# Optimization experiments

Hardware: AMD Instinct MI355X
Metric: run time of the kernel (lower is better)

Reference implementation:

```python
import jax, jax.numpy as jnp
import numpy as np
import math

HIDDEN = 768
HEADS = 12
HEAD_DIM = HIDDEN // HEADS
B, T = 2, 2048


def setup_inputs() -> dict:
    key = jax.random.key(0)
    k1, k2, k3, k4, k5 = jax.random.split(key, 5)
    s = 0.02
    return {
        "x": jax.random.normal(k1, (B, T, HIDDEN), dtype=jnp.float32),
        "mask": jnp.ones((B, T), dtype=jnp.int32),
        "w_qkv": jax.random.normal(k2, (3 * HIDDEN, HIDDEN), dtype=jnp.float32) * s,
        "b_qkv": jnp.zeros((3 * HIDDEN,), dtype=jnp.float32),
        "w_out": jax.random.normal(k3, (HIDDEN, HIDDEN), dtype=jnp.float32) * s,
        "b_out": jnp.zeros((HIDDEN,), dtype=jnp.float32),
    }


def reference(x, mask, w_qkv, b_qkv, w_out, b_out):
    Bv, Tv, C = x.shape
    # torch Linear: y = x @ W.T + b
    qkv = jnp.einsum('btc,oc->bto', x, w_qkv) + b_qkv  # [B,T,3C]
    q, k, v = jnp.split(qkv, 3, axis=-1)
    def to_heads(t):
        return t.reshape(Bv, Tv, HEADS, HEAD_DIM).transpose(0, 2, 1, 3)  # [B,H,T,D]
    q, k, v = to_heads(q), to_heads(k), to_heads(v)
    scale = 1.0 / math.sqrt(HEAD_DIM)
    scores = jnp.einsum('bhqd,bhkd->bhqk', q, k) * scale  # [B,H,T,T]
    m = (mask[:, None, None, :] != 0)  # broadcast over heads and query dim
    scores = jnp.where(m, scores, -jnp.inf)
    probs = jax.nn.softmax(scores, axis=-1)
    # dropout is identity in eval mode
    ctx = jnp.einsum('bhqk,bhkd->bhqd', probs, v)  # [B,H,T,D]
    ctx = ctx.transpose(0, 2, 1, 3).reshape(Bv, Tv, C)
    return jnp.einsum('btc,oc->bto', ctx, w_out) + b_out
```

## Files before the change

### kernel.cpp

```cpp
#include <hip/hip_runtime.h>
#include <hip/hip_bf16.h>


typedef __bf16 bf16;
typedef __attribute__((ext_vector_type(4))) __bf16 bf16x4;
typedef __attribute__((ext_vector_type(8))) __bf16 bf16x8;
typedef __attribute__((ext_vector_type(4))) float f32x4;
typedef __attribute__((ext_vector_type(16))) float f32x16;
typedef __attribute__((ext_vector_type(4))) unsigned u32x4;

#define MFMA16(a, b, c) __builtin_amdgcn_mfma_f32_16x16x32_bf16((a), (b), (c), 0, 0, 0)
#define MFMA32(a, b, c) __builtin_amdgcn_mfma_f32_32x32x16_bf16((a), (b), (c), 0, 0, 0)

static constexpr int BB = 2;
static constexpr int TT = 2048;
static constexpr int CC = 768;
static constexpr int HH = 12;
static constexpr int DD = 64;

union U8 { u32x4 u; bf16x8 b; };

__device__ inline void gload16(const bf16* g, bf16* l) {
  __builtin_amdgcn_global_load_lds((const __attribute__((address_space(1))) void*)g,
                                   (__attribute__((address_space(3))) void*)l, 16, 0, 0);
}

__global__ __launch_bounds__(256) void cvt_all(const float* __restrict__ x,
                                               const float* __restrict__ wq,
                                               const float* __restrict__ wo,
                                               bf16* __restrict__ xb,
                                               bf16* __restrict__ wqb,
                                               bf16* __restrict__ wob) {
  const int CX = BB * TT * CC / 8, CQ = 3 * CC * CC / 8;
  int idx = blockIdx.x * 256 + threadIdx.x;
  const float* s;
  bf16* d;
  int off;
  if (idx < CX) { s = x; d = xb; off = idx; }
  else if (idx < CX + CQ) { s = wq; d = wqb; off = idx - CX; }
  else { s = wo; d = wob; off = idx - CX - CQ; }
  const float4* p = (const float4*)(s + (size_t)off * 8);
  float4 a = p[0], b = p[1];
  bf16x8 r;
  r[0] = (bf16)a.x; r[1] = (bf16)a.y; r[2] = (bf16)a.z; r[3] = (bf16)a.w;
  r[4] = (bf16)b.x; r[5] = (bf16)b.y; r[6] = (bf16)b.z; r[7] = (bf16)b.w;
  *(bf16x8*)(d + (size_t)off * 8) = r;
}

template <typename OT>
__global__ __launch_bounds__(256) void gemm_bt_bf16(const bf16* __restrict__ A,
                                                    const bf16* __restrict__ Bw,
                                                    const float* __restrict__ bias,
                                                    OT* __restrict__ Cmat,
                                                    int M, int N, int K,
                                                    float qs, int qcols) {
  __shared__ bf16 As[128 * 64];
  __shared__ bf16 Bs[128 * 64];
  const int tid = threadIdx.x;
  const int m0 = blockIdx.y * 128, n0 = blockIdx.x * 128;
  const int lane = tid & 63, w = tid >> 6;
  const int wm = (w >> 1) * 64, wn = (w & 1) * 64;
  const int lr = lane & 15;
  const int g4 = lane >> 4;
  const int srow8 = lane >> 3;
  const int scs = ((lane & 7) ^ srow8) * 8;
  f32x4 acc[4][4] = {};
  for (int k0 = 0; k0 < K; k0 += 64) {
    __syncthreads();
#pragma unroll
    for (int s = 0; s < 4; s++) {
      const int rowl = w * 32 + s * 8;
      gload16(A  + (size_t)(m0 + rowl + srow8) * K + k0 + scs, &As[rowl * 64]);
      gload16(Bw + (size_t)(n0 + rowl + srow8) * K + k0 + scs, &Bs[rowl * 64]);
    }
    __syncthreads();
#pragma unroll
    for (int ks = 0; ks < 2; ks++) {
      bf16x8 a[4], b[4];
#pragma unroll
      for (int i = 0; i < 4; i++)
        a[i] = *(const bf16x8*)&As[(wm + i * 16 + lr) * 64 + (((ks * 4 + g4) ^ (lr & 7)) * 8)];
#pragma unroll
      for (int j = 0; j < 4; j++)
        b[j] = *(const bf16x8*)&Bs[(wn + j * 16 + lr) * 64 + (((ks * 4 + g4) ^ (lr & 7)) * 8)];
#pragma unroll
      for (int i = 0; i < 4; i++)
#pragma unroll
        for (int j = 0; j < 4; j++)
          acc[i][j] = MFMA16(a[i], b[j], acc[i][j]);
    }
  }
#pragma unroll
  for (int i = 0; i < 4; i++) {
    const int rbase = m0 + wm + i * 16 + (lane >> 4) * 4;
#pragma unroll
    for (int j = 0; j < 4; j++) {
      const int cidx = n0 + wn + j * 16 + lr;
      const float bv = bias[cidx];
      const float sc = (cidx < qcols) ? qs : 1.0f;
#pragma unroll
      for (int r = 0; r < 4; r++) {
        float v = (acc[i][j][r] + bv) * sc;
        Cmat[(size_t)(rbase + r) * N + cidx] = (OT)v;
      }
    }
  }
}

template <int NS>
__global__ __launch_bounds__(256, 4) void attn_fwd(const bf16* __restrict__ qkv,
                                                   const int* __restrict__ mask,
                                                   bf16* __restrict__ po,
                                                   float* __restrict__ ml,
                                                   bf16* __restrict__ ctx) {
  __shared__ bf16 Ks[2][32 * 64];
  __shared__ bf16 Vt[2][64 * 32];
  const int tid = threadIdx.x, lane = tid & 63, w = tid >> 6;
  const int ln31 = lane & 31, hi = lane >> 5;
  const int cpx = 48 * NS;
  const int bid = blockIdx.x;
  const int wg = (bid & 7) * cpx + (bid >> 3);
  const int qb = wg & 15;
  const int t2 = wg >> 4;
  const int s = t2 % NS;
  const int bh = t2 / NS;
  const int h = bh % HH, b = bh / HH;
  const int q = qb * 128 + w * 32 + ln31;
  const size_t rs = 3 * CC;
  const float NEG = -1.0e30f;
  const int kt0 = s * (TT / NS), kt1 = kt0 + TT / NS;

  bf16x8 qreg[4];
  {
    const bf16* qp = qkv + (size_t)(b * TT + q) * rs + h * DD + hi * 8;
#pragma unroll
    for (int ds = 0; ds < 4; ds++) qreg[ds] = *(const bf16x8*)(qp + ds * 16);
  }

  const bf16* kbase = qkv + (size_t)(b * TT) * rs + CC + h * DD;
  const bf16* vbase = qkv + (size_t)(b * TT) * rs + 2 * CC + h * DD;

  const int kkey = w * 8 + (lane >> 3);
  const int kcs = (lane & 7) ^ (kkey & 7) ^ (kkey >> 3);
  auto stage_k = [&](int buf, int kt) {
    gload16(kbase + (size_t)(kt + kkey) * rs + kcs * 8, &Ks[buf][w * 512]);
  };

  const int vkey = w * 8 + (lane >> 3);
  const int vd0 = (lane & 7) * 8;
  const int vpar = vkey & 1;
  const int vkp = vkey >> 1;
  bf16x8 vreg;
  int mv;
  auto load_v = [&](int kt) {
    vreg = *(const bf16x8*)(vbase + (size_t)(kt + vkey) * rs + vd0);
    mv = mask[b * TT + kt + ln31];
  };
  auto vt_put = [&](int buf, int d, unsigned val) {
    const int cp = (vkp >> 2) ^ (d & 3) ^ ((d >> 2) & 3);
    *(unsigned*)&Vt[buf][d * 32 + cp * 8 + (vkp & 3) * 2] = val;
  };
  auto write_v = [&](int buf) {
    U8 uu; uu.b = vreg;
    const u32x4 wv = uu.u;
    unsigned x0 = vpar ? wv[0] : wv[2];
    unsigned x1 = vpar ? wv[1] : wv[3];
    unsigned r0 = __shfl_xor(x0, 8);
    unsigned r1 = __shfl_xor(x1, 8);
    unsigned a0 = vpar ? r0 : wv[0];
    unsigned a1 = vpar ? r1 : wv[1];
    unsigned b0 = vpar ? wv[2] : r0;
    unsigned b1 = vpar ? wv[3] : r1;
    const int dbase = vd0 + vpar * 4;
    vt_put(buf, dbase + 0, (a0 & 0xffffu) | (b0 << 16));
    vt_put(buf, dbase + 1, (a0 >> 16) | (b0 & 0xffff0000u));
    vt_put(buf, dbase + 2, (a1 & 0xffffu) | (b1 << 16));
    vt_put(buf, dbase + 3, (a1 >> 16) | (b1 & 0xffff0000u));
  };

  stage_k(0, kt0);
  load_v(kt0);
  write_v(0);
  __syncthreads();
  int mvc = mv;

  f32x16 oacc0 = {}, oacc1 = {};
  float m = NEG, l = 0.f;
  const int swr = (ln31 & 7) ^ (ln31 >> 3);
  const int vsw = (ln31 & 3) ^ ((ln31 >> 2) & 3);

  int cur = 0;
  for (int kt = kt0; kt < kt1; kt += 32, cur ^= 1) {
    const bool more = kt + 32 < kt1;
    if (more) { stage_k(cur ^ 1, kt + 32); load_v(kt + 32); }

    f32x16 sacc = {};
    __builtin_amdgcn_s_setprio(1);
#pragma unroll
    for (int ds = 0; ds < 4; ds++) {
      bf16x8 kf = *(const bf16x8*)&Ks[cur][ln31 * 64 + ((ds * 2 + hi) ^ swr) * 8];
      sacc = MFMA32(kf, qreg[ds], sacc);
    }
    __builtin_amdgcn_s_setprio(0);

    const unsigned mw = (unsigned)__ballot(mvc != 0);
    if (mw != 0xffffffffu) {
      const unsigned mwh = mw >> (4 * hi);
#pragma unroll
      for (int r = 0; r < 16; r++) {
        const int key = (r & 3) + 8 * (r >> 2);
        if (!((mwh >> key) & 1)) sacc[r] = NEG;
      }
    }

    float mx = sacc[0];
#pragma unroll
    for (int r = 1; r < 16; r++) mx = fmaxf(mx, sacc[r]);
    mx = fmaxf(mx, __shfl_xor(mx, 32));
    if (!__all(mx - m <= 8.f)) {
      const float al = exp2f(m - mx);
      l *= al;
#pragma unroll
      for (int r = 0; r < 16; r++) { oacc0[r] *= al; oacc1[r] *= al; }
      m = mx;
    }
    float p[16], rsum = 0.f;
#pragma unroll
    for (int r = 0; r < 16; r++) { p[r] = exp2f(sacc[r] - m); rsum += p[r]; }
    rsum += __shfl_xor(rsum, 32);
    l += rsum;

    unsigned pk[8];
#pragma unroll
    for (int i = 0; i < 8; i++)
      asm("v_cvt_pk_bf16_f32 %0, %1, %2" : "=v"(pk[i]) : "v"(p[2 * i]), "v"(p[2 * i + 1]));
    asm volatile("v_permlane32_swap_b32 %0, %1" : "+v"(pk[0]), "+v"(pk[2]));
    asm volatile("v_permlane32_swap_b32 %0, %1" : "+v"(pk[1]), "+v"(pk[3]));
    asm volatile("v_permlane32_swap_b32 %0, %1" : "+v"(pk[4]), "+v"(pk[6]));
    asm volatile("v_permlane32_swap_b32 %0, %1" : "+v"(pk[5]), "+v"(pk[7]));

    __builtin_amdgcn_s_setprio(1);
#pragma unroll
    for (int ks = 0; ks < 2; ks++) {
      U8 uu;
      uu.u = (u32x4){pk[ks * 4 + 0], pk[ks * 4 + 1], pk[ks * 4 + 2], pk[ks * 4 + 3]};
      const bf16x8 pb = uu.b;
      const int cph = ((ks * 2 + hi) ^ vsw) * 8;
      bf16x8 vf0 = *(const bf16x8*)&Vt[cur][ln31 * 32 + cph];
      oacc0 = MFMA32(vf0, pb, oacc0);
      bf16x8 vf1 = *(const bf16x8*)&Vt[cur][(32 + ln31) * 32 + cph];
      oacc1 = MFMA32(vf1, pb, oacc1);
    }
    __builtin_amdgcn_s_setprio(0);

    if (more) write_v(cur ^ 1);
    __syncthreads();
    mvc = mv;
  }

  const float invl = l > 0.f ? 1.0f / l : 0.f;
  const size_t gr = (size_t)(b * TT + q);
  bf16* obase = (NS == 1) ? (ctx + gr * CC + h * DD)
                          : (po + (size_t)s * (BB * TT * CC) + gr * CC + h * DD);
#pragma unroll
  for (int g = 0; g < 4; g++) {
    bf16x4 o0, o1;
#pragma unroll
    for (int j = 0; j < 4; j++) {
      o0[j] = (bf16)(oacc0[4 * g + j] * invl);
      o1[j] = (bf16)(oacc1[4 * g + j] * invl);
    }
    *(bf16x4*)(obase + 8 * g + 4 * hi) = o0;
    *(bf16x4*)(obase + 32 + 8 * g + 4 * hi) = o1;
  }
  if (NS > 1 && hi == 0) {
    float2 v2 = {m, l};
    *(float2*)&ml[(((size_t)s * (BB * TT) + gr) * HH + h) * 2] = v2;
  }
}

template <int NS>
__global__ __launch_bounds__(256) void combine(const bf16* __restrict__ po,
                                               const float* __restrict__ ml,
                                               bf16* __restrict__ ctx) {
  const int idx = blockIdx.x * 256 + threadIdx.x;
  const int row = idx / 96;
  const int rem = idx - row * 96;
  const int h = rem >> 3, d8 = rem & 7;
  float ms[NS], ls[NS];
  float M = -1.0e30f;
#pragma unroll
  for (int s = 0; s < NS; s++) {
    const float2 p2 = *(const float2*)&ml[(((size_t)s * (BB * TT) + row) * HH + h) * 2];
    ms[s] = p2.x; ls[s] = p2.y;
    M = fmaxf(M, p2.x);
  }
  float wgt[NS], wsum = 0.f;
#pragma unroll
  for (int s = 0; s < NS; s++) { wgt[s] = ls[s] * exp2f(ms[s] - M); wsum += wgt[s]; }
  const float inv = wsum > 0.f ? 1.0f / wsum : 0.f;
  float acc[8] = {};
#pragma unroll
  for (int s = 0; s < NS; s++) {
    const float ws = wgt[s] * inv;
    const bf16x8 v = *(const bf16x8*)&po[(size_t)s * (BB * TT * CC) + (size_t)row * CC + h * 64 + d8 * 8];
#pragma unroll
    for (int j = 0; j < 8; j++) acc[j] += ws * (float)v[j];
  }
  bf16x8 o;
#pragma unroll
  for (int j = 0; j < 8; j++) o[j] = (bf16)acc[j];
  *(bf16x8*)&ctx[(size_t)row * CC + h * 64 + d8 * 8] = o;
}

extern "C" void kernel_launch(void* const* d_in, const int* in_sizes, int n_in,
                              void* d_out, int out_size, void* d_ws, size_t ws_size,
                              hipStream_t stream) {
  const float* x     = (const float*)d_in[0];
  const int*   mask  = (const int*)d_in[1];
  const float* w_qkv = (const float*)d_in[2];
  const float* b_qkv = (const float*)d_in[3];
  const float* w_out = (const float*)d_in[4];
  const float* b_out = (const float*)d_in[5];
  float* out = (float*)d_out;

  const int M = BB * TT;
  bf16* qkv = (bf16*)d_ws;
  bf16* xb  = qkv + (size_t)M * 3 * CC;
  bf16* ctx = xb;
  bf16* wob = xb + (size_t)M * CC;
  bf16* wqb = wob + (size_t)CC * CC;
  const size_t PO_OFF = (size_t)((M * 3 * CC) + (M * CC) + (CC * CC)) * 2;
  const size_t PER_SPLIT = (size_t)M * CC * 2 + (size_t)M * HH * 2 * 4;

  int NS = 1;
  if (ws_size >= PO_OFF + 8 * PER_SPLIT) NS = 8;
  else if (ws_size >= PO_OFF + 4 * PER_SPLIT) NS = 4;
  else if (ws_size >= PO_OFF + 2 * PER_SPLIT) NS = 2;

  bf16* po = (bf16*)((char*)d_ws + PO_OFF);
  float* ml = (float*)((char*)d_ws + PO_OFF + (size_t)NS * M * CC * 2);

  const int nchunks = (BB * TT * CC + 3 * CC * CC + CC * CC) / 8;
  cvt_all<<<nchunks / 256, 256, 0, stream>>>(x, w_qkv, w_out, xb, wqb, wob);
  gemm_bt_bf16<bf16><<<dim3(3 * CC / 128, M / 128), 256, 0, stream>>>(
      xb, wqb, b_qkv, qkv, M, 3 * CC, CC, 0.125f * 1.44269504f, CC);
  if (NS == 8) {
    attn_fwd<8><<<dim3(384 * 8), 256, 0, stream>>>(qkv, mask, po, ml, ctx);
    combine<8><<<dim3(M * HH * 8 / 256), 256, 0, stream>>>(po, ml, ctx);
  } else if (NS == 4) {
    attn_fwd<4><<<dim3(384 * 4), 256, 0, stream>>>(qkv, mask, po, ml, ctx);
    combine<4><<<dim3(M * HH * 8 / 256), 256, 0, stream>>>(po, ml, ctx);
  } else if (NS == 2) {
    attn_fwd<2><<<dim3(384 * 2), 256, 0, stream>>>(qkv, mask, po, ml, ctx);
    combine<2><<<dim3(M * HH * 8 / 256), 256, 0, stream>>>(po, ml, ctx);
  } else {
    attn_fwd<1><<<dim3(384), 256, 0, stream>>>(qkv, mask, po, ml, ctx);
  }
  gemm_bt_bf16<float><<<dim3(CC / 128, M / 128), 256, 0, stream>>>(
      ctx, wob, b_out, out, M, CC, CC, 1.0f, 0);
}
```

Baseline: 119.9 us.

## Prepack mask bits, drop split count to four, remap GEMM tiles, use pointer increments

Packs the int mask into 32-bit words inside the conversion kernel, so the attention loop loads one word per tile instead of doing a per-lane mask load and a ballot. Caps the split-K attention at four splits, down from eight, which cuts partial-output traffic and combine work but leaves fewer workgroups for parallelism. The GEMM kernels now remap block IDs in an interleaved order meant to improve L2 locality across XCDs. The attention K/V addresses become incremented pointers rather than being recomputed each iteration.

```diff
diff --git a/kernel.cpp b/kernel.cpp
--- a/kernel.cpp
+++ b/kernel.cpp
@@ -28,9 +28,21 @@
 __global__ __launch_bounds__(256) void cvt_all(const float* __restrict__ x,
                                                const float* __restrict__ wq,
                                                const float* __restrict__ wo,
+                                               const int* __restrict__ mask,
                                                bf16* __restrict__ xb,
                                                bf16* __restrict__ wqb,
-                                               bf16* __restrict__ wob) {
+                                               bf16* __restrict__ wob,
+                                               unsigned* __restrict__ mbits) {
+  if (blockIdx.x == gridDim.x - 1) {
+    const int i = threadIdx.x;
+    if (i < BB * TT / 32) {
+      unsigned wrd = 0;
+#pragma unroll
+      for (int j = 0; j < 32; j++) wrd |= (mask[i * 32 + j] != 0 ? 1u : 0u) << j;
+      mbits[i] = wrd;
+    }
+    return;
+  }
   const int CX = BB * TT * CC / 8, CQ = 3 * CC * CC / 8;
   int idx = blockIdx.x * 256 + threadIdx.x;
   const float* s;
@@ -57,7 +69,10 @@
   __shared__ bf16 As[128 * 64];
   __shared__ bf16 Bs[128 * 64];
   const int tid = threadIdx.x;
-  const int m0 = blockIdx.y * 128, n0 = blockIdx.x * 128;
+  const int lin = blockIdx.x + gridDim.x * blockIdx.y;
+  const int chunk = (gridDim.x * gridDim.y) >> 3;
+  const int wgid = (lin & 7) * chunk + (lin >> 3);
+  const int m0 = (wgid / gridDim.x) * 128, n0 = (wgid % gridDim.x) * 128;
   const int lane = tid & 63, w = tid >> 6;
   const int wm = (w >> 1) * 64, wn = (w & 1) * 64;
   const int lr = lane & 15;
@@ -109,7 +124,7 @@
 
 template <int NS>
 __global__ __launch_bounds__(256, 4) void attn_fwd(const bf16* __restrict__ qkv,
-                                                   const int* __restrict__ mask,
+                                                   const unsigned* __restrict__ mbits,
                                                    bf16* __restrict__ po,
                                                    float* __restrict__ ml,
                                                    bf16* __restrict__ ctx) {
@@ -128,7 +143,8 @@
   const int q = qb * 128 + w * 32 + ln31;
   const size_t rs = 3 * CC;
   const float NEG = -1.0e30f;
-  const int kt0 = s * (TT / NS), kt1 = kt0 + TT / NS;
+  const int kt0 = s * (TT / NS);
+  const int NT = (TT / NS) / 32;
 
   bf16x8 qreg[4];
   {
@@ -137,25 +153,18 @@
     for (int ds = 0; ds < 4; ds++) qreg[ds] = *(const bf16x8*)(qp + ds * 16);
   }
 
-  const bf16* kbase = qkv + (size_t)(b * TT) * rs + CC + h * DD;
-  const bf16* vbase = qkv + (size_t)(b * TT) * rs + 2 * CC + h * DD;
-
   const int kkey = w * 8 + (lane >> 3);
   const int kcs = (lane & 7) ^ (kkey & 7) ^ (kkey >> 3);
-  auto stage_k = [&](int buf, int kt) {
-    gload16(kbase + (size_t)(kt + kkey) * rs + kcs * 8, &Ks[buf][w * 512]);
-  };
+  const bf16* kpt = qkv + (size_t)(b * TT + kt0 + kkey) * rs + CC + h * DD + kcs * 8;
 
   const int vkey = w * 8 + (lane >> 3);
   const int vd0 = (lane & 7) * 8;
   const int vpar = vkey & 1;
   const int vkp = vkey >> 1;
+  const bf16* vpt = qkv + (size_t)(b * TT + kt0 + vkey) * rs + 2 * CC + h * DD + vd0;
+  const size_t stride = (size_t)32 * rs;
+
   bf16x8 vreg;
-  int mv;
-  auto load_v = [&](int kt) {
-    vreg = *(const bf16x8*)(vbase + (size_t)(kt + vkey) * rs + vd0);
-    mv = mask[b * TT + kt + ln31];
-  };
   auto vt_put = [&](int buf, int d, unsigned val) {
     const int cp = (vkp >> 2) ^ (d & 3) ^ ((d >> 2) & 3);
     *(unsigned*)&Vt[buf][d * 32 + cp * 8 + (vkp & 3) * 2] = val;
@@ -178,11 +187,14 @@
     vt_put(buf, dbase + 3, (a1 >> 16) | (b1 & 0xffff0000u));
   };
 
-  stage_k(0, kt0);
-  load_v(kt0);
+  const int mbase = (b * TT + kt0) >> 5;
+  unsigned mwc = mbits[mbase];
+
+  gload16(kpt, &Ks[0][w * 512]);
+  vreg = *(const bf16x8*)vpt;
   write_v(0);
+  kpt += stride; vpt += stride;
   __syncthreads();
-  int mvc = mv;
 
   f32x16 oacc0 = {}, oacc1 = {};
   float m = NEG, l = 0.f;
@@ -190,9 +202,15 @@
   const int vsw = (ln31 & 3) ^ ((ln31 >> 2) & 3);
 
   int cur = 0;
-  for (int kt = kt0; kt < kt1; kt += 32, cur ^= 1) {
-    const bool more = kt + 32 < kt1;
-    if (more) { stage_k(cur ^ 1, kt + 32); load_v(kt + 32); }
+  for (int it = 0; it < NT; ++it, cur ^= 1) {
+    const bool more = (it + 1 < NT);
+    unsigned mwn = 0xffffffffu;
+    if (more) {
+      gload16(kpt, &Ks[cur ^ 1][w * 512]);
+      vreg = *(const bf16x8*)vpt;
+      kpt += stride; vpt += stride;
+      mwn = mbits[mbase + it + 1];
+    }
 
     f32x16 sacc = {};
     __builtin_amdgcn_s_setprio(1);
@@ -203,13 +221,11 @@
     }
     __builtin_amdgcn_s_setprio(0);
 
-    const unsigned mw = (unsigned)__ballot(mvc != 0);
-    if (mw != 0xffffffffu) {
-      const unsigned mwh = mw >> (4 * hi);
+    if (mwc != 0xffffffffu) {
 #pragma unroll
       for (int r = 0; r < 16; r++) {
-        const int key = (r & 3) + 8 * (r >> 2);
-        if (!((mwh >> key) & 1)) sacc[r] = NEG;
+        const int key = (r & 3) + 8 * (r >> 2) + 4 * hi;
+        if (!((mwc >> key) & 1)) sacc[r] = NEG;
       }
     }
 
@@ -255,7 +271,7 @@
 
     if (more) write_v(cur ^ 1);
     __syncthreads();
-    mvc = mv;
+    mwc = mwn;
   }
 
   const float invl = l > 0.f ? 1.0f / l : 0.f;
@@ -334,28 +350,25 @@
   const size_t PER_SPLIT = (size_t)M * CC * 2 + (size_t)M * HH * 2 * 4;
 
   int NS = 1;
-  if (ws_size >= PO_OFF + 8 * PER_SPLIT) NS = 8;
-  else if (ws_size >= PO_OFF + 4 * PER_SPLIT) NS = 4;
-  else if (ws_size >= PO_OFF + 2 * PER_SPLIT) NS = 2;
+  if (ws_size >= PO_OFF + 4 * PER_SPLIT + 512) NS = 4;
+  else if (ws_size >= PO_OFF + 2 * PER_SPLIT + 512) NS = 2;
 
   bf16* po = (bf16*)((char*)d_ws + PO_OFF);
   float* ml = (float*)((char*)d_ws + PO_OFF + (size_t)NS * M * CC * 2);
+  unsigned* mbits = (unsigned*)((char*)d_ws + PO_OFF + (size_t)NS * PER_SPLIT);
 
   const int nchunks = (BB * TT * CC + 3 * CC * CC + CC * CC) / 8;
-  cvt_all<<<nchunks / 256, 256, 0, stream>>>(x, w_qkv, w_out, xb, wqb, wob);
+  cvt_all<<<nchunks / 256 + 1, 256, 0, stream>>>(x, w_qkv, w_out, mask, xb, wqb, wob, mbits);
   gemm_bt_bf16<bf16><<<dim3(3 * CC / 128, M / 128), 256, 0, stream>>>(
       xb, wqb, b_qkv, qkv, M, 3 * CC, CC, 0.125f * 1.44269504f, CC);
-  if (NS == 8) {
-    attn_fwd<8><<<dim3(384 * 8), 256, 0, stream>>>(qkv, mask, po, ml, ctx);
-    combine<8><<<dim3(M * HH * 8 / 256), 256, 0, stream>>>(po, ml, ctx);
-  } else if (NS == 4) {
-    attn_fwd<4><<<dim3(384 * 4), 256, 0, stream>>>(qkv, mask, po, ml, ctx);
+  if (NS == 4) {
+    attn_fwd<4><<<dim3(384 * 4), 256, 0, stream>>>(qkv, mbits, po, ml, ctx);
     combine<4><<<dim3(M * HH * 8 / 256), 256, 0, stream>>>(po, ml, ctx);
   } else if (NS == 2) {
-    attn_fwd<2><<<dim3(384 * 2), 256, 0, stream>>>(qkv, mask, po, ml, ctx);
+    attn_fwd<2><<<dim3(384 * 2), 256, 0, stream>>>(qkv, mbits, po, ml, ctx);
     combine<2><<<dim3(M * HH * 8 / 256), 256, 0, stream>>>(po, ml, ctx);
   } else {
-    attn_fwd<1><<<dim3(384), 256, 0, stream>>>(qkv, mask, po, ml, ctx);
+    attn_fwd<1><<<dim3(384), 256, 0, stream>>>(qkv, mbits, po, ml, ctx);
   }
   gemm_bt_bf16<float><<<dim3(CC / 128, M / 128), 256, 0, stream>>>(
       ctx, wob, b_out, out, M, CC, CC, 1.0f, 0);
```

Measured after the change: 110.9 us. -7.6%, faster.
